# Optimization experiments

Hardware: AMD Instinct MI355X
Metric: run time of the kernel (lower is better)

The kernel has to match this reference:

```python
import jax, jax.numpy as jnp
import numpy as np

PI = float(np.pi)


def setup_inputs() -> dict:
    key = jax.random.key(0)
    ks = jax.random.split(key, 12)
    B, S, D, H = 2, 2048, 512, 8
    s = 0.02
    return {
        "q": jax.random.normal(ks[0], (B, S, D), dtype=jnp.float32),
        "k": jax.random.normal(ks[1], (B, S, D), dtype=jnp.float32),
        "v": jax.random.normal(ks[2], (B, S, D), dtype=jnp.float32),
        "xdiff": jax.random.normal(ks[3], (B, S, S), dtype=jnp.float32),
        "Wq": jax.random.normal(ks[4], (D, D), dtype=jnp.float32) * s,
        "bq": jnp.zeros((D,), jnp.float32),
        "Wk": jax.random.normal(ks[5], (D, D), dtype=jnp.float32) * s,
        "bk": jnp.zeros((D,), jnp.float32),
        "Wv": jax.random.normal(ks[6], (D, D), dtype=jnp.float32) * s,
        "bv": jnp.zeros((D,), jnp.float32),
        # 10 stacked Dense(d_model -> num_heads) layers: a,b,c,d,e,f,g,h,i,j
        "Wcoef": jax.random.normal(ks[7], (10, D, H), dtype=jnp.float32) * s,
        "bcoef": jnp.zeros((10, H), jnp.float32),
        "Wo": jax.random.normal(ks[8], (D, D), dtype=jnp.float32) * s,
        "bo": jnp.zeros((D,), jnp.float32),
    }


def reference(q, k, v, xdiff, Wq, bq, Wk, bk, Wv, bv, Wcoef, bcoef, Wo, bo):
    B, S, D = q.shape
    H = Wcoef.shape[-1]
    dh = D // H

    qp = q @ Wq + bq            # (B,S,D)
    kp = k @ Wk + bk
    vp = v @ Wv + bv

    # 10 per-head scalar coefficients computed from the projected queries.
    # coefs: (10, B, H, Sq)
    coefs = jnp.einsum('bsd,ndh->nbhs', qp, Wcoef) + bcoef[:, None, :, None]
    # term 2 uses -0.5*|b|*x^2: abs goes on the coefficient, -0.5 into the basis
    coefs = coefs.at[1].set(jnp.abs(coefs[1]))

    x = xdiff                   # (B, Sq, Sk)
    basis = jnp.stack([
        x,
        -0.5 * x * x,
        jnp.sin(PI * x), jnp.cos(PI * x),
        jnp.sin(3 * PI * x), jnp.cos(3 * PI * x),
        jnp.sin(5 * PI * x), jnp.cos(5 * PI * x),
        jnp.sin(9 * PI * x), jnp.cos(9 * PI * x),
    ])                          # (10, B, Sq, Sk)

    initial_logits = 0.1 * jnp.einsum('nbhq,nbqk->bhqk', coefs, basis)  # (B,H,Sq,Sk)

    qh = qp.reshape(B, S, H, dh).transpose(0, 2, 1, 3)  # (B,H,S,dh)
    kh = kp.reshape(B, S, H, dh).transpose(0, 2, 1, 3)
    vh = vp.reshape(B, S, H, dh).transpose(0, 2, 1, 3)

    logits = (jnp.einsum('bhqd,bhkd->bhqk', qh, kh) + initial_logits) \
             / jnp.sqrt(jnp.asarray(dh, qp.dtype))
    attn = jax.nn.softmax(logits, axis=-1)              # (B,H,Sq,Sk)

    out = jnp.einsum('bhqk,bhkd->bqhd', attn, vh).reshape(B, S, D)
    out = out @ Wo + bo
    return (out, attn)
```

## Files before the change

kernel.cpp:

```cpp
#include <hip/hip_runtime.h>

typedef unsigned short u16;
typedef unsigned int u32;
typedef __attribute__((ext_vector_type(8))) short s16x8;
typedef __attribute__((ext_vector_type(4))) float f32x4;

#define PIf 3.14159265358979323846f

__device__ __forceinline__ float bf2f(u16 u) {
    unsigned v = (unsigned)u << 16;
    return __builtin_bit_cast(float, v);
}
__device__ __forceinline__ u16 f2bf(float f) {
    unsigned u = __builtin_bit_cast(unsigned, f);
    u += 0x7fffu + ((u >> 16) & 1u);
    return (u16)(u >> 16);
}
__device__ __forceinline__ float b2f_lo(unsigned w) { return __builtin_bit_cast(float, w << 16); }
__device__ __forceinline__ float b2f_hi(unsigned w) { return __builtin_bit_cast(float, w & 0xffff0000u); }

#define OFF_FLAG 0
#define OFF_WT   256
#define OFF_WCT  2097408
#define OFF_QB   2179328
#define OFF_KB   6373632
#define OFF_VB   10567936
#define OFF_XB   14762240
#define OFF_QP   31539456
#define OFF_KP   35733760
#define OFF_VP   39928064
#define OFF_VT   44122368
#define OFF_COEF 48316672
#define OFF_CTX  49627392
#define OFF_BIAS 53821696
#define OFF_INV  53829888
#define OFF_PBUF 53960960

__global__ void kdetect(const u32* __restrict__ wq, int* __restrict__ flag) {
    int lane = threadIdx.x;
    float v = fabsf(__builtin_bit_cast(float, wq[lane]));
    bool smallv = (v > 1e-30f) && (v < 0.5f);
    unsigned long long m = __ballot(smallv);
    if (lane == 0) *flag = (__popcll(m) >= 32) ? 1 : 0;
}

__global__ void kcvt(const void* __restrict__ src, u16* __restrict__ dst, int n,
                     const int* __restrict__ flag) {
    int i = (blockIdx.x * 256 + threadIdx.x) * 4;
    if (i >= n) return;
    if (*flag) {
        float4 f = *(const float4*)((const float*)src + i);
        u16 r[4] = {f2bf(f.x), f2bf(f.y), f2bf(f.z), f2bf(f.w)};
        *(uint2*)(dst + i) = *(const uint2*)r;
    } else {
        *(uint2*)(dst + i) = *(const uint2*)((const u16*)src + i);
    }
}

__global__ void kbias(const void* __restrict__ bq, const void* __restrict__ bk,
                      const void* __restrict__ bv, const void* __restrict__ bo,
                      const void* __restrict__ bc, u16* __restrict__ dst,
                      const int* __restrict__ flag) {
    int t = threadIdx.x;
    bool f = *flag != 0;
    dst[t]        = f ? f2bf(((const float*)bq)[t]) : ((const u16*)bq)[t];
    dst[512 + t]  = f ? f2bf(((const float*)bk)[t]) : ((const u16*)bk)[t];
    dst[1024 + t] = f ? f2bf(((const float*)bv)[t]) : ((const u16*)bv)[t];
    dst[1536 + t] = f ? f2bf(((const float*)bo)[t]) : ((const u16*)bo)[t];
    if (t < 80)
        dst[2048 + t] = f ? f2bf(((const float*)bc)[t]) : ((const u16*)bc)[t];
}

__global__ void ktrans512(const void* __restrict__ wq, const void* __restrict__ wk,
                          const void* __restrict__ wv, const void* __restrict__ wo,
                          u16* __restrict__ dst, const int* __restrict__ flag) {
    __shared__ u16 t[32][33];
    const void* srcs[4] = {wq, wk, wv, wo};
    const void* src = srcs[blockIdx.z];
    bool f = *flag != 0;
    u16* d = dst + (size_t)blockIdx.z * 512 * 512;
    int x0 = blockIdx.x * 32, y0 = blockIdx.y * 32;
    size_t si = (size_t)(y0 + threadIdx.y) * 512 + x0 + threadIdx.x;
    t[threadIdx.y][threadIdx.x] = f ? f2bf(((const float*)src)[si]) : ((const u16*)src)[si];
    __syncthreads();
    d[(size_t)(x0 + threadIdx.y) * 512 + y0 + threadIdx.x] = t[threadIdx.x][threadIdx.y];
}

__global__ void kwct(const void* __restrict__ wc, u16* __restrict__ dst,
                     const int* __restrict__ flag) {
    int nh = blockIdx.x;
    int n = nh >> 3, h = nh & 7;
    bool f = *flag != 0;
    for (int d = threadIdx.x; d < 512; d += 64) {
        size_t si = ((size_t)n * 512 + d) * 8 + h;
        dst[nh * 512 + d] = f ? f2bf(((const float*)wc)[si]) : ((const u16*)wc)[si];
    }
}

__global__ __launch_bounds__(256) void kgemm(const u16* __restrict__ A, const u16* __restrict__ BT,
                                             const u16* __restrict__ bias, u16* __restrict__ out) {
    __shared__ u16 As[64][40];
    __shared__ u16 Bs[64][40];
    int tid = threadIdx.x;
    int w = tid >> 6, lane = tid & 63, quad = lane >> 4, col = lane & 15;
    int m0 = blockIdx.y * 64, n0 = blockIdx.x * 64;
    int wm = (w >> 1) * 32, wn = (w & 1) * 32;
    int sr = tid >> 2, sc = tid & 3;
    f32x4 acc[2][2] = {};
    for (int kt = 0; kt < 512; kt += 32) {
        __syncthreads();
        *(uint4*)&As[sr][sc * 8] = *(const uint4*)&A[(size_t)(m0 + sr) * 512 + kt + sc * 8];
        *(uint4*)&Bs[sr][sc * 8] = *(const uint4*)&BT[(size_t)(n0 + sr) * 512 + kt + sc * 8];
        __syncthreads();
        s16x8 a[2], b[2];
        a[0] = *(const s16x8*)&As[wm + col][quad * 8];
        a[1] = *(const s16x8*)&As[wm + 16 + col][quad * 8];
        b[0] = *(const s16x8*)&Bs[wn + col][quad * 8];
        b[1] = *(const s16x8*)&Bs[wn + 16 + col][quad * 8];
#pragma unroll
        for (int mi = 0; mi < 2; mi++)
#pragma unroll
            for (int ni = 0; ni < 2; ni++)
                acc[mi][ni] = __builtin_amdgcn_mfma_f32_16x16x32_bf16(a[mi], b[ni], acc[mi][ni], 0, 0, 0);
    }
#pragma unroll
    for (int mi = 0; mi < 2; mi++)
#pragma unroll
        for (int ni = 0; ni < 2; ni++) {
            int n = n0 + wn + ni * 16 + col;
            float bv = bf2f(bias[n]);
#pragma unroll
            for (int r = 0; r < 4; r++) {
                int m = m0 + wm + mi * 16 + quad * 4 + r;
                out[(size_t)m * 512 + n] = f2bf(acc[mi][ni][r] + bv);
            }
        }
}

template <int F32>
__global__ __launch_bounds__(256) void kgemm_final(const u16* __restrict__ A, const u16* __restrict__ BT,
                                                   const u16* __restrict__ bias, u16* __restrict__ outH,
                                                   float* __restrict__ outF, const int* __restrict__ flag) {
    if (*flag != F32) return;
    __shared__ u16 As[64][40];
    __shared__ u16 Bs[64][40];
    int tid = threadIdx.x;
    int w = tid >> 6, lane = tid & 63, quad = lane >> 4, col = lane & 15;
    int m0 = blockIdx.y * 64, n0 = blockIdx.x * 64;
    int wm = (w >> 1) * 32, wn = (w & 1) * 32;
    int sr = tid >> 2, sc = tid & 3;
    f32x4 acc[2][2] = {};
    for (int kt = 0; kt < 512; kt += 32) {
        __syncthreads();
        *(uint4*)&As[sr][sc * 8] = *(const uint4*)&A[(size_t)(m0 + sr) * 512 + kt + sc * 8];
        *(uint4*)&Bs[sr][sc * 8] = *(const uint4*)&BT[(size_t)(n0 + sr) * 512 + kt + sc * 8];
        __syncthreads();
        s16x8 a[2], b[2];
        a[0] = *(const s16x8*)&As[wm + col][quad * 8];
        a[1] = *(const s16x8*)&As[wm + 16 + col][quad * 8];
        b[0] = *(const s16x8*)&Bs[wn + col][quad * 8];
        b[1] = *(const s16x8*)&Bs[wn + 16 + col][quad * 8];
#pragma unroll
        for (int mi = 0; mi < 2; mi++)
#pragma unroll
            for (int ni = 0; ni < 2; ni++)
                acc[mi][ni] = __builtin_amdgcn_mfma_f32_16x16x32_bf16(a[mi], b[ni], acc[mi][ni], 0, 0, 0);
    }
#pragma unroll
    for (int mi = 0; mi < 2; mi++)
#pragma unroll
        for (int ni = 0; ni < 2; ni++) {
            int n = n0 + wn + ni * 16 + col;
            float bv = bf2f(bias[n]);
#pragma unroll
            for (int r = 0; r < 4; r++) {
                int m = m0 + wm + mi * 16 + quad * 4 + r;
                float val = acc[mi][ni][r] + bv;
                if constexpr (F32) outF[(size_t)m * 512 + n] = val;
                else               outH[(size_t)m * 512 + n] = f2bf(val);
            }
        }
}

__global__ void kvtrans(const u16* __restrict__ vp, u16* __restrict__ vT) {
    __shared__ u16 t[32][33];
    int b = blockIdx.z;
    int d0 = blockIdx.x * 32, s0 = blockIdx.y * 32;
    t[threadIdx.y][threadIdx.x] = vp[((size_t)b * 2048 + s0 + threadIdx.y) * 512 + d0 + threadIdx.x];
    __syncthreads();
    vT[((size_t)b * 512 + d0 + threadIdx.y) * 2048 + s0 + threadIdx.x] = t[threadIdx.x][threadIdx.y];
}

__global__ __launch_bounds__(256) void kcoef(const u16* __restrict__ qp, const u16* __restrict__ wct,
                                             const u16* __restrict__ bc, float* __restrict__ cout) {
    __shared__ u16 As[64][40];
    int tid = threadIdx.x;
    int w = tid >> 6, lane = tid & 63, quad = lane >> 4, col = lane & 15;
    int m0 = blockIdx.x * 64;
    int sr = tid >> 2, sc = tid & 3;
    f32x4 acc[5] = {};
    for (int kt = 0; kt < 512; kt += 32) {
        __syncthreads();
        *(uint4*)&As[sr][sc * 8] = *(const uint4*)&qp[(size_t)(m0 + sr) * 512 + kt + sc * 8];
        __syncthreads();
        s16x8 a = *(const s16x8*)&As[w * 16 + col][quad * 8];
#pragma unroll
        for (int nt = 0; nt < 5; nt++) {
            uint4 bv4 = *(const uint4*)&wct[(size_t)(nt * 16 + col) * 512 + kt + quad * 8];
            acc[nt] = __builtin_amdgcn_mfma_f32_16x16x32_bf16(a, __builtin_bit_cast(s16x8, bv4), acc[nt], 0, 0, 0);
        }
    }
    int m = m0 + w * 16 + quad * 4;
    int b = m >> 11, s = m & 2047;
#pragma unroll
    for (int nt = 0; nt < 5; nt++) {
        int nh = nt * 16 + col, n = nh >> 3, h = nh & 7;
        float bvv = bf2f(bc[nh]);
        float4 o;
        float tmp[4];
#pragma unroll
        for (int r = 0; r < 4; r++) {
            float c = acc[nt][r] + bvv;
            if (n == 1) c = fabsf(c);
            tmp[r] = c * 0.0125f;
        }
        o.x = tmp[0]; o.y = tmp[1]; o.z = tmp[2]; o.w = tmp[3];
        *(float4*)&cout[((size_t)((b * 8 + h) * 10 + n)) * 2048 + s] = o;
    }
}

template <int MODE>
__global__ __launch_bounds__(256) void kattn_f(const u16* __restrict__ qp, const u16* __restrict__ kp,
                                               const u16* __restrict__ vT, const u16* __restrict__ xd,
                                               const float* __restrict__ coef,
                                               u16* __restrict__ p16, float* __restrict__ p32,
                                               u16* __restrict__ ctx, float* __restrict__ invb,
                                               const int* __restrict__ flag) {
    if constexpr (MODE == 0) { if (*flag != 0) return; }
    else                     { if (*flag != 1) return; }
    __shared__ u16 qs[64][72];
    __shared__ u16 ks[128][72];
    __shared__ u16 xs[64][136];
    __shared__ float cfl[10][64];

    int tid = threadIdx.x;
    int w = tid >> 6, lane = tid & 63, quad = lane >> 4, col = lane & 15;
    int qt = blockIdx.x, bh = blockIdx.y;
    int b = bh >> 3, h = bh & 7;
    int q0 = qt * 64;

    {
        int r = tid >> 2, qu = tid & 3;
        const u16* src = qp + ((size_t)(b * 2048 + q0 + r)) * 512 + h * 64 + qu * 16;
        *(uint4*)&qs[r][qu * 16] = *(const uint4*)&src[0];
        *(uint4*)&qs[r][qu * 16 + 8] = *(const uint4*)&src[8];
    }
    if (tid < 160) {
        int n = tid >> 4, i = tid & 15;
        *(float4*)&cfl[n][i * 4] = *(const float4*)&coef[((size_t)(bh * 10 + n)) * 2048 + q0 + i * 4];
    }
    __syncthreads();

    float cf[40];
#pragma unroll
    for (int n = 0; n < 10; n++)
#pragma unroll
        for (int r = 0; r < 4; r++) cf[n * 4 + r] = cfl[n][w * 16 + quad * 4 + r];

    s16x8 a0 = *(const s16x8*)&qs[w * 16 + col][quad * 8];
    s16x8 a1 = *(const s16x8*)&qs[w * 16 + col][32 + quad * 8];

    float s_l[4] = {0.f, 0.f, 0.f, 0.f};
    f32x4 accv[4] = {};

    size_t abase = ((size_t)(bh * 2048 + q0)) * 2048;
    const u16* vb0 = vT + ((size_t)(b * 512 + h * 64 + col)) * 2048 + quad * 8;

    for (int k0 = 0; k0 < 2048; k0 += 128) {
        __syncthreads();
        {
            int kr = tid >> 1, hf = tid & 1;
            const u16* src = kp + ((size_t)(b * 2048 + k0 + kr)) * 512 + h * 64 + hf * 32;
#pragma unroll
            for (int i = 0; i < 4; i++) *(uint4*)&ks[kr][hf * 32 + i * 8] = *(const uint4*)&src[i * 8];
        }
        {
            int qr = tid >> 2, qu = tid & 3;
            const u16* src = xd + ((size_t)(b * 2048 + q0 + qr)) * 2048 + k0 + qu * 32;
#pragma unroll
            for (int i = 0; i < 4; i++) *(uint4*)&xs[qr][qu * 32 + i * 8] = *(const uint4*)&src[i * 8];
        }
        __syncthreads();
#pragma unroll
        for (int nt = 0; nt < 8; nt++) {
            s16x8 b0 = *(const s16x8*)&ks[nt * 16 + col][quad * 8];
            s16x8 b1 = *(const s16x8*)&ks[nt * 16 + col][32 + quad * 8];
            f32x4 acc = {0.f, 0.f, 0.f, 0.f};
            acc = __builtin_amdgcn_mfma_f32_16x16x32_bf16(a0, b0, acc, 0, 0, 0);
            acc = __builtin_amdgcn_mfma_f32_16x16x32_bf16(a1, b1, acc, 0, 0, 0);
#pragma unroll
            for (int r = 0; r < 4; r++) {
                int lq = w * 16 + quad * 4 + r;
                int kk = nt * 16 + col;
                float x = bf2f(xs[lq][kk]);
                float ang = PIf * x;
                float s1 = __sinf(ang), c1 = __cosf(ang);
                float s2 = 2.f * s1 * c1, c2 = 1.f - 2.f * s1 * s1;
                float s3 = s1 * c2 + c1 * s2, c3 = c1 * c2 - s1 * s2;
                float s5 = s3 * c2 + c3 * s2, c5 = c3 * c2 - s3 * s2;
                float s4 = 2.f * s2 * c2, c4 = 1.f - 2.f * s2 * s2;
                float s9 = s5 * c4 + c5 * s4, c9 = c5 * c4 - s5 * s4;
                float dot = cf[0 * 4 + r] * x + cf[1 * 4 + r] * (-0.5f * x * x)
                          + cf[2 * 4 + r] * s1 + cf[3 * 4 + r] * c1
                          + cf[4 * 4 + r] * s3 + cf[5 * 4 + r] * c3
                          + cf[6 * 4 + r] * s5 + cf[7 * 4 + r] * c5
                          + cf[8 * 4 + r] * s9 + cf[9 * 4 + r] * c9;
                float logit = acc[r] * 0.125f + dot;
                float p = __expf(logit);
                size_t idx = abase + (size_t)lq * 2048 + k0 + kk;
                u16 pb = f2bf(p);
                if constexpr (MODE == 2) p32[idx] = p;
                else                     p16[idx] = pb;
                s_l[r] += p;
                xs[lq][kk] = pb;
            }
        }
#pragma unroll
        for (int kc = 0; kc < 4; kc++) {
            s16x8 af = *(const s16x8*)&xs[w * 16 + col][kc * 32 + quad * 8];
#pragma unroll
            for (int nt = 0; nt < 4; nt++) {
                uint4 bv4 = *(const uint4*)&vb0[(size_t)nt * 16 * 2048 + k0 + kc * 32];
                accv[nt] = __builtin_amdgcn_mfma_f32_16x16x32_bf16(af, __builtin_bit_cast(s16x8, bv4), accv[nt], 0, 0, 0);
            }
        }
    }

    float inv_r[4];
#pragma unroll
    for (int r = 0; r < 4; r++) {
        float s = s_l[r];
#pragma unroll
        for (int off = 1; off < 16; off <<= 1) s += __shfl_xor(s, off);
        inv_r[r] = 1.f / s;
    }
    if (col == 0) {
#pragma unroll
        for (int r = 0; r < 4; r++)
            invb[bh * 2048 + q0 + w * 16 + quad * 4 + r] = inv_r[r];
    }
#pragma unroll
    for (int nt = 0; nt < 4; nt++)
#pragma unroll
        for (int r = 0; r < 4; r++) {
            int q = q0 + w * 16 + quad * 4 + r;
            int d = h * 64 + nt * 16 + col;
            ctx[((size_t)(b * 2048 + q)) * 512 + d] = f2bf(accv[nt][r] * inv_r[r]);
        }
}

template <int MODE>
__global__ __launch_bounds__(256) void knorm(u16* __restrict__ p16, float* __restrict__ p32,
                                             const float* __restrict__ invb, const int* __restrict__ flag) {
    if constexpr (MODE == 0) { if (*flag != 0) return; }
    else                     { if (*flag != 1) return; }
    int row = blockIdx.x;
    float inv = invb[row];
    size_t base = (size_t)row * 2048 + threadIdx.x * 8;
    if constexpr (MODE == 0) {
        uint4 vv = *(const uint4*)&p16[base];
        unsigned a[4] = {vv.x, vv.y, vv.z, vv.w};
#pragma unroll
        for (int i = 0; i < 4; i++) {
            float lo = b2f_lo(a[i]) * inv;
            float hi = b2f_hi(a[i]) * inv;
            a[i] = ((unsigned)f2bf(hi) << 16) | (unsigned)f2bf(lo);
        }
        uint4 o; o.x = a[0]; o.y = a[1]; o.z = a[2]; o.w = a[3];
        *(uint4*)&p16[base] = o;
    } else if constexpr (MODE == 1) {
        uint4 vv = *(const uint4*)&p16[base];
        unsigned a[4] = {vv.x, vv.y, vv.z, vv.w};
        float4 o0, o1;
        o0.x = b2f_lo(a[0]) * inv; o0.y = b2f_hi(a[0]) * inv;
        o0.z = b2f_lo(a[1]) * inv; o0.w = b2f_hi(a[1]) * inv;
        o1.x = b2f_lo(a[2]) * inv; o1.y = b2f_hi(a[2]) * inv;
        o1.z = b2f_lo(a[3]) * inv; o1.w = b2f_hi(a[3]) * inv;
        *(float4*)&p32[base] = o0;
        *(float4*)&p32[base + 4] = o1;
    } else {
        float4 v0 = *(const float4*)&p32[base];
        float4 v1 = *(const float4*)&p32[base + 4];
        v0.x *= inv; v0.y *= inv; v0.z *= inv; v0.w *= inv;
        v1.x *= inv; v1.y *= inv; v1.z *= inv; v1.w *= inv;
        *(float4*)&p32[base] = v0;
        *(float4*)&p32[base + 4] = v1;
    }
}

extern "C" void kernel_launch(void* const* d_in, const int* in_sizes, int n_in,
                              void* d_out, int out_size, void* d_ws, size_t ws_size,
                              hipStream_t stream) {
    const void* q  = d_in[0];
    const void* k  = d_in[1];
    const void* v  = d_in[2];
    const void* xd = d_in[3];
    const void* Wq = d_in[4];
    const void* bq = d_in[5];
    const void* Wk = d_in[6];
    const void* bk = d_in[7];
    const void* Wv = d_in[8];
    const void* bv = d_in[9];
    const void* Wc = d_in[10];
    const void* bc = d_in[11];
    const void* Wo = d_in[12];
    const void* bo = d_in[13];

    char* ws = (char*)d_ws;
    int*   flag = (int*)(ws + OFF_FLAG);
    u16*   WT   = (u16*)(ws + OFF_WT);
    u16*   WcT  = (u16*)(ws + OFF_WCT);
    u16*   qb   = (u16*)(ws + OFF_QB);
    u16*   kb   = (u16*)(ws + OFF_KB);
    u16*   vb   = (u16*)(ws + OFF_VB);
    u16*   xb   = (u16*)(ws + OFF_XB);
    u16*   qp   = (u16*)(ws + OFF_QP);
    u16*   kp   = (u16*)(ws + OFF_KP);
    u16*   vp   = (u16*)(ws + OFF_VP);
    u16*   vT   = (u16*)(ws + OFF_VT);
    float* coef = (float*)(ws + OFF_COEF);
    u16*   ctx  = (u16*)(ws + OFF_CTX);
    u16*   bB   = (u16*)(ws + OFF_BIAS);
    float* invb = (float*)(ws + OFF_INV);
    u16*   pbuf = (u16*)(ws + OFF_PBUF);

    u16*   outH  = (u16*)d_out;
    u16*   attnH = outH + 2097152;
    float* outF  = (float*)d_out;
    float* attnF = outF + 2097152;

    bool big = ws_size >= (size_t)OFF_PBUF + 134217728ull;

    kdetect<<<1, 64, 0, stream>>>((const u32*)Wq, flag);
    kcvt<<<2048, 256, 0, stream>>>(q, qb, 2097152, flag);
    kcvt<<<2048, 256, 0, stream>>>(k, kb, 2097152, flag);
    kcvt<<<2048, 256, 0, stream>>>(v, vb, 2097152, flag);
    kcvt<<<8192, 256, 0, stream>>>(xd, xb, 8388608, flag);
    kbias<<<1, 512, 0, stream>>>(bq, bk, bv, bo, bc, bB, flag);
    ktrans512<<<dim3(16, 16, 4), dim3(32, 32), 0, stream>>>(Wq, Wk, Wv, Wo, WT, flag);
    kwct<<<80, 64, 0, stream>>>(Wc, WcT, flag);
    kgemm<<<dim3(8, 64), 256, 0, stream>>>(qb, WT, bB, qp);
    kgemm<<<dim3(8, 64), 256, 0, stream>>>(kb, WT + 262144, bB + 512, kp);
    kgemm<<<dim3(8, 64), 256, 0, stream>>>(vb, WT + 524288, bB + 1024, vp);
    kvtrans<<<dim3(16, 64, 2), dim3(32, 32), 0, stream>>>(vp, vT);
    kcoef<<<64, 256, 0, stream>>>(qp, WcT, bB + 2048, coef);

    kattn_f<0><<<dim3(32, 16), 256, 0, stream>>>(qp, kp, vT, xb, coef, attnH, attnF, ctx, invb, flag);
    if (big)
        kattn_f<1><<<dim3(32, 16), 256, 0, stream>>>(qp, kp, vT, xb, coef, pbuf, attnF, ctx, invb, flag);
    else
        kattn_f<2><<<dim3(32, 16), 256, 0, stream>>>(qp, kp, vT, xb, coef, attnH, attnF, ctx, invb, flag);

    knorm<0><<<32768, 256, 0, stream>>>(attnH, attnF, invb, flag);
    if (big)
        knorm<1><<<32768, 256, 0, stream>>>(pbuf, attnF, invb, flag);
    else
        knorm<2><<<32768, 256, 0, stream>>>(attnH, attnF, invb, flag);

    kgemm_final<0><<<dim3(8, 64), 256, 0, stream>>>(ctx, WT + 786432, bB + 1536, outH, outF, flag);
    kgemm_final<1><<<dim3(8, 64), 256, 0, stream>>>(ctx, WT + 786432, bB + 1536, outH, outF, flag);
}
```

Before: 652.8 us.

## Split attention key tiles across 8 waves and merge launches per dtype

The attention kernel now runs 512 threads per block. Waves are split into 4 row groups by 2 key-column halves, and the two halves' PV accumulators and row sums are combined through shared memory at the end. The q/k/v conversions are merged into one launch, and the per-flag duplicate launches of the attention, norm and final GEMM kernels are collapsed so fewer empty launches run. The goal is more waves per CU to hide latency in the compute-heavy attention loop and less launch overhead. The cost is an extra shared-memory reduction and possibly higher register pressure under launch_bounds(512).

```diff
diff --git a/kernel.cpp b/kernel.cpp
--- a/kernel.cpp
+++ b/kernel.cpp
@@ -44,6 +44,22 @@
     if (lane == 0) *flag = (__popcll(m) >= 32) ? 1 : 0;
 }
 
+__global__ void kcvt3(const void* __restrict__ s0, const void* __restrict__ s1,
+                      const void* __restrict__ s2, u16* __restrict__ dst,
+                      const int* __restrict__ flag) {
+    const void* srcs[3] = {s0, s1, s2};
+    const void* src = srcs[blockIdx.y];
+    u16* d = dst + (size_t)blockIdx.y * 2097152;
+    int i = (blockIdx.x * 256 + threadIdx.x) * 4;
+    if (*flag) {
+        float4 f = *(const float4*)((const float*)src + i);
+        u16 r[4] = {f2bf(f.x), f2bf(f.y), f2bf(f.z), f2bf(f.w)};
+        *(uint2*)(d + i) = *(const uint2*)r;
+    } else {
+        *(uint2*)(d + i) = *(const uint2*)((const u16*)src + i);
+    }
+}
+
 __global__ void kcvt(const void* __restrict__ src, u16* __restrict__ dst, int n,
                      const int* __restrict__ flag) {
     int i = (blockIdx.x * 256 + threadIdx.x) * 4;
@@ -137,11 +153,10 @@
         }
 }
 
-template <int F32>
 __global__ __launch_bounds__(256) void kgemm_final(const u16* __restrict__ A, const u16* __restrict__ BT,
                                                    const u16* __restrict__ bias, u16* __restrict__ outH,
                                                    float* __restrict__ outF, const int* __restrict__ flag) {
-    if (*flag != F32) return;
+    bool f32o = *flag != 0;
     __shared__ u16 As[64][40];
     __shared__ u16 Bs[64][40];
     int tid = threadIdx.x;
@@ -176,8 +191,8 @@
             for (int r = 0; r < 4; r++) {
                 int m = m0 + wm + mi * 16 + quad * 4 + r;
                 float val = acc[mi][ni][r] + bv;
-                if constexpr (F32) outF[(size_t)m * 512 + n] = val;
-                else               outH[(size_t)m * 512 + n] = f2bf(val);
+                if (f32o) outF[(size_t)m * 512 + n] = val;
+                else      outH[(size_t)m * 512 + n] = f2bf(val);
             }
         }
 }
@@ -229,31 +244,36 @@
     }
 }
 
-template <int MODE>
-__global__ __launch_bounds__(256) void kattn_f(const u16* __restrict__ qp, const u16* __restrict__ kp,
+template <int F32S>
+__global__ __launch_bounds__(512) void kattn_t(const u16* __restrict__ qp, const u16* __restrict__ kp,
                                                const u16* __restrict__ vT, const u16* __restrict__ xd,
                                                const float* __restrict__ coef,
-                                               u16* __restrict__ p16, float* __restrict__ p32,
+                                               u16* __restrict__ attnH, u16* __restrict__ pbuf,
+                                               float* __restrict__ p32,
                                                u16* __restrict__ ctx, float* __restrict__ invb,
-                                               const int* __restrict__ flag) {
-    if constexpr (MODE == 0) { if (*flag != 0) return; }
-    else                     { if (*flag != 1) return; }
+                                               const int* __restrict__ flag, int big) {
+    int fl = *flag;
+    if constexpr (F32S) { if (fl != 1) return; }
+    else                { if (fl && !big) return; }
+    u16* p16 = fl ? pbuf : attnH;
+
     __shared__ u16 qs[64][72];
     __shared__ u16 ks[128][72];
     __shared__ u16 xs[64][136];
     __shared__ float cfl[10][64];
 
     int tid = threadIdx.x;
-    int w = tid >> 6, lane = tid & 63, quad = lane >> 4, col = lane & 15;
+    int lane = tid & 63, quad = lane >> 4, col = lane & 15;
+    int w = tid >> 6;
+    int wr = w & 3, wc = w >> 2;
     int qt = blockIdx.x, bh = blockIdx.y;
     int b = bh >> 3, h = bh & 7;
     int q0 = qt * 64;
 
     {
-        int r = tid >> 2, qu = tid & 3;
-        const u16* src = qp + ((size_t)(b * 2048 + q0 + r)) * 512 + h * 64 + qu * 16;
-        *(uint4*)&qs[r][qu * 16] = *(const uint4*)&src[0];
-        *(uint4*)&qs[r][qu * 16 + 8] = *(const uint4*)&src[8];
+        int r = tid >> 3, qu = tid & 7;
+        const u16* src = qp + ((size_t)(b * 2048 + q0 + r)) * 512 + h * 64 + qu * 8;
+        *(uint4*)&qs[r][qu * 8] = *(const uint4*)src;
     }
     if (tid < 160) {
         int n = tid >> 4, i = tid & 15;
@@ -265,10 +285,10 @@
 #pragma unroll
     for (int n = 0; n < 10; n++)
 #pragma unroll
-        for (int r = 0; r < 4; r++) cf[n * 4 + r] = cfl[n][w * 16 + quad * 4 + r];
-
-    s16x8 a0 = *(const s16x8*)&qs[w * 16 + col][quad * 8];
-    s16x8 a1 = *(const s16x8*)&qs[w * 16 + col][32 + quad * 8];
+        for (int r = 0; r < 4; r++) cf[n * 4 + r] = cfl[n][wr * 16 + quad * 4 + r];
+
+    s16x8 a0 = *(const s16x8*)&qs[wr * 16 + col][quad * 8];
+    s16x8 a1 = *(const s16x8*)&qs[wr * 16 + col][32 + quad * 8];
 
     float s_l[4] = {0.f, 0.f, 0.f, 0.f};
     f32x4 accv[4] = {};
@@ -279,29 +299,30 @@
     for (int k0 = 0; k0 < 2048; k0 += 128) {
         __syncthreads();
         {
-            int kr = tid >> 1, hf = tid & 1;
-            const u16* src = kp + ((size_t)(b * 2048 + k0 + kr)) * 512 + h * 64 + hf * 32;
-#pragma unroll
-            for (int i = 0; i < 4; i++) *(uint4*)&ks[kr][hf * 32 + i * 8] = *(const uint4*)&src[i * 8];
+            int kr = tid >> 2, hf = tid & 3;
+            const u16* src = kp + ((size_t)(b * 2048 + k0 + kr)) * 512 + h * 64 + hf * 16;
+            *(uint4*)&ks[kr][hf * 16]     = *(const uint4*)&src[0];
+            *(uint4*)&ks[kr][hf * 16 + 8] = *(const uint4*)&src[8];
         }
         {
-            int qr = tid >> 2, qu = tid & 3;
-            const u16* src = xd + ((size_t)(b * 2048 + q0 + qr)) * 2048 + k0 + qu * 32;
-#pragma unroll
-            for (int i = 0; i < 4; i++) *(uint4*)&xs[qr][qu * 32 + i * 8] = *(const uint4*)&src[i * 8];
-        }
-        __syncthreads();
-#pragma unroll
-        for (int nt = 0; nt < 8; nt++) {
-            s16x8 b0 = *(const s16x8*)&ks[nt * 16 + col][quad * 8];
-            s16x8 b1 = *(const s16x8*)&ks[nt * 16 + col][32 + quad * 8];
+            int qr = tid >> 3, qu = tid & 7;
+            const u16* src = xd + ((size_t)(b * 2048 + q0 + qr)) * 2048 + k0 + qu * 16;
+            *(uint4*)&xs[qr][qu * 16]     = *(const uint4*)&src[0];
+            *(uint4*)&xs[qr][qu * 16 + 8] = *(const uint4*)&src[8];
+        }
+        __syncthreads();
+#pragma unroll
+        for (int nt = 0; nt < 4; nt++) {
+            int ntg = wc * 4 + nt;
+            s16x8 b0 = *(const s16x8*)&ks[ntg * 16 + col][quad * 8];
+            s16x8 b1 = *(const s16x8*)&ks[ntg * 16 + col][32 + quad * 8];
             f32x4 acc = {0.f, 0.f, 0.f, 0.f};
             acc = __builtin_amdgcn_mfma_f32_16x16x32_bf16(a0, b0, acc, 0, 0, 0);
             acc = __builtin_amdgcn_mfma_f32_16x16x32_bf16(a1, b1, acc, 0, 0, 0);
 #pragma unroll
             for (int r = 0; r < 4; r++) {
-                int lq = w * 16 + quad * 4 + r;
-                int kk = nt * 16 + col;
+                int lq = wr * 16 + quad * 4 + r;
+                int kk = ntg * 16 + col;
                 float x = bf2f(xs[lq][kk]);
                 float ang = PIf * x;
                 float s1 = __sinf(ang), c1 = __cosf(ang);
@@ -319,15 +340,16 @@
                 float p = __expf(logit);
                 size_t idx = abase + (size_t)lq * 2048 + k0 + kk;
                 u16 pb = f2bf(p);
-                if constexpr (MODE == 2) p32[idx] = p;
-                else                     p16[idx] = pb;
+                if constexpr (F32S) p32[idx] = p;
+                else                p16[idx] = pb;
                 s_l[r] += p;
                 xs[lq][kk] = pb;
             }
         }
 #pragma unroll
-        for (int kc = 0; kc < 4; kc++) {
-            s16x8 af = *(const s16x8*)&xs[w * 16 + col][kc * 32 + quad * 8];
+        for (int kc2 = 0; kc2 < 2; kc2++) {
+            int kc = wc * 2 + kc2;
+            s16x8 af = *(const s16x8*)&xs[wr * 16 + col][kc * 32 + quad * 8];
 #pragma unroll
             for (int nt = 0; nt < 4; nt++) {
                 uint4 bv4 = *(const uint4*)&vb0[(size_t)nt * 16 * 2048 + k0 + kc * 32];
@@ -336,39 +358,62 @@
         }
     }
 
-    float inv_r[4];
+    float sred[4];
 #pragma unroll
     for (int r = 0; r < 4; r++) {
         float s = s_l[r];
 #pragma unroll
         for (int off = 1; off < 16; off <<= 1) s += __shfl_xor(s, off);
-        inv_r[r] = 1.f / s;
-    }
-    if (col == 0) {
+        sred[r] = s;
+    }
+
+    __syncthreads();
+    float* red  = (float*)&ks[0][0];
+    float* psum = (float*)&xs[0][0];
+    if (wc == 1) {
+#pragma unroll
+        for (int nt = 0; nt < 4; nt++)
+#pragma unroll
+            for (int r = 0; r < 4; r++)
+                red[(wr * 64 + lane) * 16 + nt * 4 + r] = accv[nt][r];
+        if (col == 0) {
+#pragma unroll
+            for (int r = 0; r < 4; r++) psum[wr * 16 + quad * 4 + r] = sred[r];
+        }
+    }
+    __syncthreads();
+    if (wc == 0) {
+        float inv_r[4];
 #pragma unroll
         for (int r = 0; r < 4; r++)
-            invb[bh * 2048 + q0 + w * 16 + quad * 4 + r] = inv_r[r];
-    }
-#pragma unroll
-    for (int nt = 0; nt < 4; nt++)
-#pragma unroll
-        for (int r = 0; r < 4; r++) {
-            int q = q0 + w * 16 + quad * 4 + r;
-            int d = h * 64 + nt * 16 + col;
-            ctx[((size_t)(b * 2048 + q)) * 512 + d] = f2bf(accv[nt][r] * inv_r[r]);
-        }
-}
-
-template <int MODE>
-__global__ __launch_bounds__(256) void knorm(u16* __restrict__ p16, float* __restrict__ p32,
+            inv_r[r] = 1.f / (sred[r] + psum[wr * 16 + quad * 4 + r]);
+        if (col == 0) {
+#pragma unroll
+            for (int r = 0; r < 4; r++)
+                invb[bh * 2048 + q0 + wr * 16 + quad * 4 + r] = inv_r[r];
+        }
+#pragma unroll
+        for (int nt = 0; nt < 4; nt++)
+#pragma unroll
+            for (int r = 0; r < 4; r++) {
+                float vsum = accv[nt][r] + red[(wr * 64 + lane) * 16 + nt * 4 + r];
+                int q = q0 + wr * 16 + quad * 4 + r;
+                int d = h * 64 + nt * 16 + col;
+                ctx[((size_t)(b * 2048 + q)) * 512 + d] = f2bf(vsum * inv_r[r]);
+            }
+    }
+}
+
+template <int BIG>
+__global__ __launch_bounds__(256) void knorm(u16* __restrict__ attnH, const u16* __restrict__ pbuf,
+                                             float* __restrict__ attnF,
                                              const float* __restrict__ invb, const int* __restrict__ flag) {
-    if constexpr (MODE == 0) { if (*flag != 0) return; }
-    else                     { if (*flag != 1) return; }
+    int fl = *flag;
     int row = blockIdx.x;
     float inv = invb[row];
     size_t base = (size_t)row * 2048 + threadIdx.x * 8;
-    if constexpr (MODE == 0) {
-        uint4 vv = *(const uint4*)&p16[base];
+    if (fl == 0) {
+        uint4 vv = *(const uint4*)&attnH[base];
         unsigned a[4] = {vv.x, vv.y, vv.z, vv.w};
 #pragma unroll
         for (int i = 0; i < 4; i++) {
@@ -377,24 +422,24 @@
             a[i] = ((unsigned)f2bf(hi) << 16) | (unsigned)f2bf(lo);
         }
         uint4 o; o.x = a[0]; o.y = a[1]; o.z = a[2]; o.w = a[3];
-        *(uint4*)&p16[base] = o;
-    } else if constexpr (MODE == 1) {
-        uint4 vv = *(const uint4*)&p16[base];
+        *(uint4*)&attnH[base] = o;
+    } else if constexpr (BIG) {
+        uint4 vv = *(const uint4*)&pbuf[base];
         unsigned a[4] = {vv.x, vv.y, vv.z, vv.w};
         float4 o0, o1;
         o0.x = b2f_lo(a[0]) * inv; o0.y = b2f_hi(a[0]) * inv;
         o0.z = b2f_lo(a[1]) * inv; o0.w = b2f_hi(a[1]) * inv;
         o1.x = b2f_lo(a[2]) * inv; o1.y = b2f_hi(a[2]) * inv;
         o1.z = b2f_lo(a[3]) * inv; o1.w = b2f_hi(a[3]) * inv;
-        *(float4*)&p32[base] = o0;
-        *(float4*)&p32[base + 4] = o1;
+        *(float4*)&attnF[base] = o0;
+        *(float4*)&attnF[base + 4] = o1;
     } else {
-        float4 v0 = *(const float4*)&p32[base];
-        float4 v1 = *(const float4*)&p32[base + 4];
+        float4 v0 = *(const float4*)&attnF[base];
+        float4 v1 = *(const float4*)&attnF[base + 4];
         v0.x *= inv; v0.y *= inv; v0.z *= inv; v0.w *= inv;
         v1.x *= inv; v1.y *= inv; v1.z *= inv; v1.w *= inv;
-        *(float4*)&p32[base] = v0;
-        *(float4*)&p32[base + 4] = v1;
+        *(float4*)&attnF[base] = v0;
+        *(float4*)&attnF[base + 4] = v1;
     }
 }
 
@@ -442,9 +487,7 @@
     bool big = ws_size >= (size_t)OFF_PBUF + 134217728ull;
 
     kdetect<<<1, 64, 0, stream>>>((const u32*)Wq, flag);
-    kcvt<<<2048, 256, 0, stream>>>(q, qb, 2097152, flag);
-    kcvt<<<2048, 256, 0, stream>>>(k, kb, 2097152, flag);
-    kcvt<<<2048, 256, 0, stream>>>(v, vb, 2097152, flag);
+    kcvt3<<<dim3(2048, 3), 256, 0, stream>>>(q, k, v, qb, flag);
     kcvt<<<8192, 256, 0, stream>>>(xd, xb, 8388608, flag);
     kbias<<<1, 512, 0, stream>>>(bq, bk, bv, bo, bc, bB, flag);
     ktrans512<<<dim3(16, 16, 4), dim3(32, 32), 0, stream>>>(Wq, Wk, Wv, Wo, WT, flag);
@@ -455,18 +498,14 @@
     kvtrans<<<dim3(16, 64, 2), dim3(32, 32), 0, stream>>>(vp, vT);
     kcoef<<<64, 256, 0, stream>>>(qp, WcT, bB + 2048, coef);
 
-    kattn_f<0><<<dim3(32, 16), 256, 0, stream>>>(qp, kp, vT, xb, coef, attnH, attnF, ctx, invb, flag);
-    if (big)
-        kattn_f<1><<<dim3(32, 16), 256, 0, stream>>>(qp, kp, vT, xb, coef, pbuf, attnF, ctx, invb, flag);
-    else
-        kattn_f<2><<<dim3(32, 16), 256, 0, stream>>>(qp, kp, vT, xb, coef, attnH, attnF, ctx, invb, flag);
-
-    knorm<0><<<32768, 256, 0, stream>>>(attnH, attnF, invb, flag);
-    if (big)
-        knorm<1><<<32768, 256, 0, stream>>>(pbuf, attnF, invb, flag);
-    else
-        knorm<2><<<32768, 256, 0, stream>>>(attnH, attnF, invb, flag);
-
-    kgemm_final<0><<<dim3(8, 64), 256, 0, stream>>>(ctx, WT + 786432, bB + 1536, outH, outF, flag);
-    kgemm_final<1><<<dim3(8, 64), 256, 0, stream>>>(ctx, WT + 786432, bB + 1536, outH, outF, flag);
-}
+    kattn_t<0><<<dim3(32, 16), 512, 0, stream>>>(qp, kp, vT, xb, coef, attnH, pbuf, attnF,
+                                                 ctx, invb, flag, (int)big);
+    if (!big)
+        kattn_t<1><<<dim3(32, 16), 512, 0, stream>>>(qp, kp, vT, xb, coef, attnH, pbuf, attnF,
+                                                     ctx, invb, flag, 0);
+
+    if (big) knorm<1><<<32768, 256, 0, stream>>>(attnH, pbuf, attnF, invb, flag);
+    else     knorm<0><<<32768, 256, 0, stream>>>(attnH, pbuf, attnF, invb, flag);
+
+    kgemm_final<<<dim3(8, 64), 256, 0, stream>>>(ctx, WT + 786432, bB + 1536, outH, outF, flag);
+}
```

Result: faster. 637.9 us (-2.3%).
